# Kernel tuning notes

Hardware: AMD Instinct MI355X
Metric: run time of the kernel (lower is better)

## Reference

```python
import jax, jax.numpy as jnp
import numpy as np

B, T, D, N, H = 2, 2048, 1024, 16, 64
CAP = 50.0


def setup_inputs() -> dict:
    key = jax.random.key(0)
    ks = jax.random.split(key, 11)
    s_in = 1.0 / np.sqrt(D)   # kaiming_uniform(a=sqrt(5)) bound for fan_in=D
    s_out = 1.0 / np.sqrt(N * H)
    return {
        "q_vector": jax.random.normal(ks[0], (B, T, D), jnp.float32),
        "k_vector": jax.random.normal(ks[1], (B, T, D), jnp.float32),
        "v_vector": jax.random.normal(ks[2], (B, T, D), jnp.float32),
        "wq": jax.random.uniform(ks[3], (D, N, H), jnp.float32, -s_in, s_in),
        "bq": jnp.zeros((N, H), jnp.float32),
        "wk": jax.random.uniform(ks[4], (D, N, H), jnp.float32, -s_in, s_in),
        "bk": jnp.zeros((N, H), jnp.float32),
        "wv": jax.random.uniform(ks[5], (D, N, H), jnp.float32, -s_in, s_in),
        "bv": jnp.zeros((N, H), jnp.float32),
        "wo": jax.random.uniform(ks[6], (N, H, D), jnp.float32, -s_out, s_out),
        "bo": jnp.zeros((D,), jnp.float32),
    }


def reference(q_vector, k_vector, v_vector, wq, bq, wk, bk, wv, bv, wo, bo):
    # QKV projections: '...D,DNH->...NH' + bias
    q = jnp.einsum("btd,dnh->btnh", q_vector, wq) + bq
    k = jnp.einsum("bsd,dnh->bsnh", k_vector, wk) + bk
    v = jnp.einsum("bsd,dnh->bsnh", v_vector, wv) + bv
    # scale query by head_dim^-0.5 (use_per_dim_scale=False path)
    q = q * (H ** -0.5)
    # logits [B,N,T,S] with tanh soft-cap
    logits = jnp.einsum("btnh,bsnh->bnts", q, k)
    logits = CAP * jnp.tanh(logits / CAP)
    probs = jax.nn.softmax(logits, axis=-1)
    encoded = jnp.einsum("bnts,bsnh->btnh", probs, v)
    # output projection: '...NH,NHD->...D' + bias
    out = jnp.einsum("btnh,nhd->btd", encoded, wo) + bo
    return (out, probs)
```

## Files before the change

### kernel.cpp

```cpp
#include <hip/hip_runtime.h>

#define BB 2
#define TT 2048
#define DD 1024
#define NN 16
#define HH 64
#define NHC 1024
#define CAPV 50.0f

typedef float f32x4 __attribute__((ext_vector_type(4)));
typedef __bf16 bf16x8 __attribute__((ext_vector_type(8)));
typedef unsigned short u16x8 __attribute__((ext_vector_type(8)));

__device__ __forceinline__ unsigned short f2bf(float f) {
  unsigned u = __builtin_bit_cast(unsigned, f);
  unsigned r = (u + 0x7fffu + ((u >> 16) & 1u)) >> 16;
  return (unsigned short)r;
}

__device__ __forceinline__ void gld16(void* lds, const void* g) {
  __builtin_amdgcn_global_load_lds(
      (__attribute__((address_space(1))) void*)(const_cast<void*>(g)),
      (__attribute__((address_space(3))) void*)(lds), 16, 0, 0);
}

__global__ __launch_bounds__(256) void conv_inputs(
    const float* __restrict__ q, const float* __restrict__ k, const float* __restrict__ v,
    unsigned short* __restrict__ qo, unsigned short* __restrict__ ko, unsigned short* __restrict__ vo) {
  const float* src = blockIdx.z == 0 ? q : (blockIdx.z == 1 ? k : v);
  unsigned short* dst = blockIdx.z == 0 ? qo : (blockIdx.z == 1 ? ko : vo);
  size_t i = ((size_t)blockIdx.x * 256 + threadIdx.x) * 8;
  float4 a = *(const float4*)&src[i];
  float4 c = *(const float4*)&src[i + 4];
  u16x8 o;
  o[0] = f2bf(a.x); o[1] = f2bf(a.y); o[2] = f2bf(a.z); o[3] = f2bf(a.w);
  o[4] = f2bf(c.x); o[5] = f2bf(c.y); o[6] = f2bf(c.z); o[7] = f2bf(c.w);
  *(u16x8*)&dst[i] = o;
}

__global__ __launch_bounds__(256) void transpose_w(
    const float* __restrict__ wq, const float* __restrict__ wk,
    const float* __restrict__ wv, const float* __restrict__ wo,
    unsigned short* __restrict__ oq, unsigned short* __restrict__ ok,
    unsigned short* __restrict__ ov, unsigned short* __restrict__ oo) {
  __shared__ float tile[64][65];
  int z = blockIdx.z;
  const float* src = z == 0 ? wq : z == 1 ? wk : z == 2 ? wv : wo;
  unsigned short* dst = z == 0 ? oq : z == 1 ? ok : z == 2 ? ov : oo;
  int r0 = blockIdx.y * 64, c0 = blockIdx.x * 64;
  int tid = threadIdx.x;
#pragma unroll
  for (int i = 0; i < 16; ++i) {
    int idx = tid + 256 * i; int r = idx >> 6, c = idx & 63;
    tile[r][c] = src[(size_t)(r0 + r) * 1024 + c0 + c];
  }
  __syncthreads();
#pragma unroll
  for (int i = 0; i < 16; ++i) {
    int idx = tid + 256 * i; int rr = idx >> 6, cc = idx & 63;
    dst[(size_t)(c0 + rr) * 1024 + r0 + cc] = f2bf(tile[cc][rr]);
  }
}

__global__ __launch_bounds__(256) void transpose_v(
    const unsigned short* __restrict__ vb, unsigned short* __restrict__ vT) {
  __shared__ unsigned short tl[64][80];
  int s0 = blockIdx.x * 64, n = blockIdx.y, b = blockIdx.z;
  int tid = threadIdx.x;
  const size_t base = (size_t)b * TT * NHC + (size_t)n * HH;
#pragma unroll
  for (int i = 0; i < 2; ++i) {
    int c = tid + 256 * i; int r = c >> 3, g = c & 7;
    *(u16x8*)&tl[r][g * 8] = *(const u16x8*)&vb[base + (size_t)(s0 + r) * NHC + g * 8];
  }
  __syncthreads();
  const size_t vtb = (size_t)(b * NN + n) * HH * TT;
#pragma unroll
  for (int i = 0; i < 2; ++i) {
    int c = tid + 256 * i; int h = c >> 3, sg = c & 7;
    u16x8 w;
#pragma unroll
    for (int j = 0; j < 8; ++j) w[j] = tl[sg * 8 + j][h];
    *(u16x8*)&vT[vtb + (size_t)h * TT + s0 + sg * 8] = w;
  }
}

template <int OUT_F32>
__global__ __launch_bounds__(256) void gemm128(
    const unsigned short* __restrict__ A, const unsigned short* __restrict__ BT,
    const float* __restrict__ bias, void* __restrict__ Cout, float scale) {
  __shared__ unsigned short As[128 * 64];
  __shared__ unsigned short Bs[128 * 64];
  const int tid = threadIdx.x, lane = tid & 63, wave = tid >> 6;
  const int wm = wave >> 1, wn = wave & 1;
  const int l15 = lane & 15, l4 = lane >> 4;
  const int row0 = blockIdx.y * 128, col0 = blockIdx.x * 128;
  f32x4 acc[4][4] = {};
  for (int kt = 0; kt < 16; ++kt) {
    if (kt) __syncthreads();
#pragma unroll
    for (int i = 0; i < 4; ++i) {
      int c = tid + 256 * i; int r = c >> 3, g = (c & 7) ^ (r & 7);
      gld16(&As[c * 8], &A[(size_t)(row0 + r) * 1024 + kt * 64 + g * 8]);
    }
#pragma unroll
    for (int i = 0; i < 4; ++i) {
      int c = tid + 256 * i; int r = c >> 3, g = (c & 7) ^ (r & 7);
      gld16(&Bs[c * 8], &BT[(size_t)(col0 + r) * 1024 + kt * 64 + g * 8]);
    }
    __syncthreads();
#pragma unroll
    for (int ks = 0; ks < 2; ++ks) {
      bf16x8 af[4], bfr[4];
#pragma unroll
      for (int m = 0; m < 4; ++m) {
        int r = wm * 64 + m * 16 + l15;
        int ch = (ks * 4 + l4) ^ (r & 7);
        af[m] = *(const bf16x8*)&As[r * 64 + ch * 8];
      }
#pragma unroll
      for (int n = 0; n < 4; ++n) {
        int r = wn * 64 + n * 16 + l15;
        int ch = (ks * 4 + l4) ^ (r & 7);
        bfr[n] = *(const bf16x8*)&Bs[r * 64 + ch * 8];
      }
#pragma unroll
      for (int m = 0; m < 4; ++m)
#pragma unroll
        for (int n = 0; n < 4; ++n)
          acc[m][n] = __builtin_amdgcn_mfma_f32_16x16x32_bf16(af[m], bfr[n], acc[m][n], 0, 0, 0);
    }
  }
#pragma unroll
  for (int m = 0; m < 4; ++m)
#pragma unroll
    for (int n = 0; n < 4; ++n) {
      int col = col0 + wn * 64 + n * 16 + l15;
      float bv = bias[col];
#pragma unroll
      for (int r = 0; r < 4; ++r) {
        int row = row0 + wm * 64 + m * 16 + l4 * 4 + r;
        float v = (acc[m][n][r] + bv) * scale;
        if (OUT_F32) ((float*)Cout)[(size_t)row * 1024 + col] = v;
        else ((unsigned short*)Cout)[(size_t)row * 1024 + col] = f2bf(v);
      }
    }
}

__global__ __launch_bounds__(256) void attn_denom(
    const unsigned short* __restrict__ qb, const unsigned short* __restrict__ kb,
    float* __restrict__ denom) {
  __shared__ unsigned short q_lds[128 * 64];
  __shared__ unsigned short k_lds[128 * 64];
  __shared__ float rs[2][128];
  const int tid = threadIdx.x, lane = tid & 63, wave = tid >> 6;
  const int wm = wave >> 1, wn = wave & 1;
  const int l15 = lane & 15, l4 = lane >> 4;
  const int t0 = blockIdx.x * 128, n = blockIdx.y, b = blockIdx.z;
  const size_t base = (size_t)b * TT * NHC + (size_t)n * HH;
#pragma unroll
  for (int i = 0; i < 4; ++i) {
    int c = tid + 256 * i; int r = c >> 3, g = (c & 7) ^ (r & 7);
    gld16(&q_lds[c * 8], &qb[base + (size_t)(t0 + r) * NHC + g * 8]);
  }
  __syncthreads();
  bf16x8 qf[4][2];
#pragma unroll
  for (int m = 0; m < 4; ++m)
#pragma unroll
    for (int ks = 0; ks < 2; ++ks) {
      int r = wm * 64 + m * 16 + l15;
      int ch = (ks * 4 + l4) ^ (r & 7);
      qf[m][ks] = *(const bf16x8*)&q_lds[r * 64 + ch * 8];
    }
  float psum[4][4] = {};
  for (int st = 0; st < 16; ++st) {
    __syncthreads();
#pragma unroll
    for (int i = 0; i < 4; ++i) {
      int c = tid + 256 * i; int r = c >> 3, g = (c & 7) ^ (r & 7);
      gld16(&k_lds[c * 8], &kb[base + (size_t)(st * 128 + r) * NHC + g * 8]);
    }
    __syncthreads();
    f32x4 acc[4][4] = {};
#pragma unroll
    for (int ks = 0; ks < 2; ++ks) {
      bf16x8 bfr[4];
#pragma unroll
      for (int nf = 0; nf < 4; ++nf) {
        int r = wn * 64 + nf * 16 + l15;
        int ch = (ks * 4 + l4) ^ (r & 7);
        bfr[nf] = *(const bf16x8*)&k_lds[r * 64 + ch * 8];
      }
#pragma unroll
      for (int m = 0; m < 4; ++m)
#pragma unroll
        for (int nf = 0; nf < 4; ++nf)
          acc[m][nf] = __builtin_amdgcn_mfma_f32_16x16x32_bf16(qf[m][ks], bfr[nf], acc[m][nf], 0, 0, 0);
    }
#pragma unroll
    for (int m = 0; m < 4; ++m)
#pragma unroll
      for (int nf = 0; nf < 4; ++nf)
#pragma unroll
        for (int r = 0; r < 4; ++r) {
          float l = acc[m][nf][r];
          float u = __expf(l * (2.0f / CAPV));
          float ct = CAPV * (u - 1.0f) * __builtin_amdgcn_rcpf(u + 1.0f);
          psum[m][r] += __expf(ct);
        }
  }
#pragma unroll
  for (int m = 0; m < 4; ++m)
#pragma unroll
    for (int r = 0; r < 4; ++r) {
      float s = psum[m][r];
      s += __shfl_xor(s, 1);
      s += __shfl_xor(s, 2);
      s += __shfl_xor(s, 4);
      s += __shfl_xor(s, 8);
      if (l15 == 0) rs[wn][wm * 64 + m * 16 + l4 * 4 + r] = s;
    }
  __syncthreads();
  if (tid < 128) denom[((size_t)b * NN + n) * TT + t0 + tid] = rs[0][tid] + rs[1][tid];
}

__global__ __launch_bounds__(256) void attn_pv(
    const unsigned short* __restrict__ qb, const unsigned short* __restrict__ kb,
    const unsigned short* __restrict__ vT, const float* __restrict__ denom,
    float* __restrict__ probs, unsigned short* __restrict__ enc) {
  __shared__ unsigned short regA[64 * 128];
  __shared__ unsigned short regB[128 * 136];
  const int tid = threadIdx.x, lane = tid & 63, wave = tid >> 6;
  const int wm = wave >> 1, wn = wave & 1;
  const int l15 = lane & 15, l4 = lane >> 4;
  const int t0 = blockIdx.x * 128, n = blockIdx.y, b = blockIdx.z;
  const size_t base = (size_t)b * TT * NHC + (size_t)n * HH;
  const size_t vtb = (size_t)(b * NN + n) * HH * TT;
  const size_t prow = (size_t)(b * NN + n) * TT;
#pragma unroll
  for (int i = 0; i < 4; ++i) {
    int c = tid + 256 * i; int r = c >> 3, g = (c & 7) ^ (r & 7);
    gld16(&regA[c * 8], &qb[base + (size_t)(t0 + r) * NHC + g * 8]);
  }
  __syncthreads();
  bf16x8 qf[4][2];
#pragma unroll
  for (int m = 0; m < 4; ++m)
#pragma unroll
    for (int ks = 0; ks < 2; ++ks) {
      int r = wm * 64 + m * 16 + l15;
      int ch = (ks * 4 + l4) ^ (r & 7);
      qf[m][ks] = *(const bf16x8*)&regA[r * 64 + ch * 8];
    }
  float dinv[4][4];
#pragma unroll
  for (int m = 0; m < 4; ++m)
#pragma unroll
    for (int r = 0; r < 4; ++r)
      dinv[m][r] = 1.0f / denom[((size_t)b * NN + n) * TT + t0 + wm * 64 + m * 16 + l4 * 4 + r];
  __syncthreads();
  f32x4 eacc[2][4] = {};
  for (int st = 0; st < 16; ++st) {
    const int s0 = st * 128;
#pragma unroll
    for (int i = 0; i < 4; ++i) {
      int c = tid + 256 * i; int r = c >> 3, g = (c & 7) ^ (r & 7);
      gld16(&regB[c * 8], &kb[base + (size_t)(s0 + r) * NHC + g * 8]);
    }
#pragma unroll
    for (int i = 0; i < 4; ++i) {
      int c = tid + 256 * i; int h = c >> 4, g = (c & 15) ^ (h & 15);
      gld16(&regA[c * 8], &vT[vtb + (size_t)h * TT + s0 + g * 8]);
    }
    __syncthreads();
    f32x4 acc[4][4] = {};
#pragma unroll
    for (int ks = 0; ks < 2; ++ks) {
      bf16x8 bfr[4];
#pragma unroll
      for (int nf = 0; nf < 4; ++nf) {
        int r = wn * 64 + nf * 16 + l15;
        int ch = (ks * 4 + l4) ^ (r & 7);
        bfr[nf] = *(const bf16x8*)&regB[r * 64 + ch * 8];
      }
#pragma unroll
      for (int m = 0; m < 4; ++m)
#pragma unroll
        for (int nf = 0; nf < 4; ++nf)
          acc[m][nf] = __builtin_amdgcn_mfma_f32_16x16x32_bf16(qf[m][ks], bfr[nf], acc[m][nf], 0, 0, 0);
    }
    __syncthreads();
#pragma unroll
    for (int m = 0; m < 4; ++m)
#pragma unroll
      for (int nf = 0; nf < 4; ++nf) {
        int scol = wn * 64 + nf * 16 + l15;
#pragma unroll
        for (int r = 0; r < 4; ++r) {
          int trow = wm * 64 + m * 16 + l4 * 4 + r;
          float l = acc[m][nf][r];
          float u = __expf(l * (2.0f / CAPV));
          float ct = CAPV * (u - 1.0f) * __builtin_amdgcn_rcpf(u + 1.0f);
          float p = __expf(ct) * dinv[m][r];
          probs[(prow + t0 + trow) * (size_t)TT + s0 + scol] = p;
          regB[trow * 136 + scol] = f2bf(p);
        }
      }
    __syncthreads();
#pragma unroll
    for (int kst = 0; kst < 4; ++kst) {
      bf16x8 pa[2], vbf[4];
#pragma unroll
      for (int m2 = 0; m2 < 2; ++m2) {
        int t = wave * 32 + m2 * 16 + l15;
        pa[m2] = *(const bf16x8*)&regB[t * 136 + kst * 32 + l4 * 8];
      }
#pragma unroll
      for (int h4 = 0; h4 < 4; ++h4) {
        int h = h4 * 16 + l15;
        int ch = (kst * 4 + l4) ^ (h & 15);
        vbf[h4] = *(const bf16x8*)&regA[h * 128 + ch * 8];
      }
#pragma unroll
      for (int m2 = 0; m2 < 2; ++m2)
#pragma unroll
        for (int h4 = 0; h4 < 4; ++h4)
          eacc[m2][h4] = __builtin_amdgcn_mfma_f32_16x16x32_bf16(pa[m2], vbf[h4], eacc[m2][h4], 0, 0, 0);
    }
    __syncthreads();
  }
#pragma unroll
  for (int m2 = 0; m2 < 2; ++m2)
#pragma unroll
    for (int h4 = 0; h4 < 4; ++h4)
#pragma unroll
      for (int r = 0; r < 4; ++r) {
        int t = t0 + wave * 32 + m2 * 16 + l4 * 4 + r;
        int h = h4 * 16 + l15;
        enc[base + (size_t)t * NHC + h] = f2bf(eacc[m2][h4][r]);
      }
}

extern "C" void kernel_launch(void* const* d_in, const int* in_sizes, int n_in,
                              void* d_out, int out_size, void* d_ws, size_t ws_size,
                              hipStream_t stream) {
  const float* qv = (const float*)d_in[0];
  const float* kv = (const float*)d_in[1];
  const float* vv = (const float*)d_in[2];
  const float* wq = (const float*)d_in[3];
  const float* bq = (const float*)d_in[4];
  const float* wk = (const float*)d_in[5];
  const float* bk = (const float*)d_in[6];
  const float* wv = (const float*)d_in[7];
  const float* bv = (const float*)d_in[8];
  const float* wo = (const float*)d_in[9];
  const float* bo = (const float*)d_in[10];
  char* ws = (char*)d_ws;
  unsigned short* qb   = (unsigned short*)(ws + 0);
  unsigned short* kb   = (unsigned short*)(ws + 8388608);
  unsigned short* vb   = (unsigned short*)(ws + 16777216);
  unsigned short* vTb  = (unsigned short*)(ws + 25165824);
  unsigned short* wqT  = (unsigned short*)(ws + 33554432);
  unsigned short* wkT  = (unsigned short*)(ws + 35651584);
  unsigned short* wvT  = (unsigned short*)(ws + 37748736);
  unsigned short* woT  = (unsigned short*)(ws + 39845888);
  unsigned short* qinb = (unsigned short*)(ws + 41943040);
  unsigned short* kinb = (unsigned short*)(ws + 50331648);
  unsigned short* vinb = (unsigned short*)(ws + 58720256);
  float* denom         = (float*)(ws + 67108864);
  unsigned short* enc  = (unsigned short*)(ws + 67371008);

  float* out = (float*)d_out;
  float* probs = out + (size_t)BB * TT * DD;

  conv_inputs<<<dim3(2048, 1, 3), 256, 0, stream>>>(qv, kv, vv, qinb, kinb, vinb);
  transpose_w<<<dim3(16, 16, 4), 256, 0, stream>>>(wq, wk, wv, wo, wqT, wkT, wvT, woT);
  gemm128<0><<<dim3(8, 32), 256, 0, stream>>>(qinb, wqT, bq, qb, 0.125f);
  gemm128<0><<<dim3(8, 32), 256, 0, stream>>>(kinb, wkT, bk, kb, 1.0f);
  gemm128<0><<<dim3(8, 32), 256, 0, stream>>>(vinb, wvT, bv, vb, 1.0f);
  transpose_v<<<dim3(32, 16, 2), 256, 0, stream>>>(vb, vTb);
  attn_denom<<<dim3(16, 16, 2), 256, 0, stream>>>(qb, kb, denom);
  attn_pv<<<dim3(16, 16, 2), 256, 0, stream>>>(qb, kb, vTb, denom, probs, enc);
  gemm128<1><<<dim3(8, 32), 256, 0, stream>>>(enc, woT, bo, out, 1.0f);
}
```

Baseline: 368.8 us.

## Fuse denominator and PV attention kernels into one sync-free per-wave kernel

Merges the two attention kernels into one launch, with a block-index remap for locality. Each wave owns 32 query rows and recomputes QK^T twice: once for the softmax denominator, once for the probabilities and PV product. K and V fragments are read straight from global memory instead of staged through shared memory, which removes all block barriers. Probabilities are packed to bf16 in a small per-wave LDS tile and written back as 16-byte vector stores, and the normalisation moves to the encoder output. The trade-offs are redundant global K/V reads across waves, and probs now derived from bf16-rounded values, which costs some precision.

```diff
diff --git a/kernel.cpp b/kernel.cpp
--- a/kernel.cpp
+++ b/kernel.cpp
@@ -147,61 +147,51 @@
     }
 }
 
-__global__ __launch_bounds__(256) void attn_denom(
+__global__ __launch_bounds__(256, 2) void fused_attn(
     const unsigned short* __restrict__ qb, const unsigned short* __restrict__ kb,
-    float* __restrict__ denom) {
-  __shared__ unsigned short q_lds[128 * 64];
-  __shared__ unsigned short k_lds[128 * 64];
-  __shared__ float rs[2][128];
+    const unsigned short* __restrict__ vT, float* __restrict__ probs,
+    unsigned short* __restrict__ enc) {
+  __shared__ unsigned short P_lds[4][32][136];
   const int tid = threadIdx.x, lane = tid & 63, wave = tid >> 6;
-  const int wm = wave >> 1, wn = wave & 1;
   const int l15 = lane & 15, l4 = lane >> 4;
-  const int t0 = blockIdx.x * 128, n = blockIdx.y, b = blockIdx.z;
+  const int bid = blockIdx.x;
+  const int logical = (bid & 7) * 64 + (bid >> 3);
+  const int bt = logical & 15, head = logical >> 4;
+  const int n = head & 15, b = head >> 4;
+  const int t0 = bt * 128;
+  const int wrow0 = t0 + wave * 32;
   const size_t base = (size_t)b * TT * NHC + (size_t)n * HH;
-#pragma unroll
-  for (int i = 0; i < 4; ++i) {
-    int c = tid + 256 * i; int r = c >> 3, g = (c & 7) ^ (r & 7);
-    gld16(&q_lds[c * 8], &qb[base + (size_t)(t0 + r) * NHC + g * 8]);
-  }
-  __syncthreads();
-  bf16x8 qf[4][2];
-#pragma unroll
-  for (int m = 0; m < 4; ++m)
+  const size_t vtb = (size_t)(b * NN + n) * HH * TT;
+  const size_t prow = (size_t)(b * NN + n) * TT;
+
+  bf16x8 qf[2][2];
+#pragma unroll
+  for (int m = 0; m < 2; ++m)
+#pragma unroll
+    for (int ks = 0; ks < 2; ++ks)
+      qf[m][ks] = *(const bf16x8*)&qb[base + (size_t)(wrow0 + m * 16 + l15) * NHC + ks * 32 + l4 * 8];
+
+  float psum[2][4] = {};
+#pragma unroll 1
+  for (int st = 0; st < 16; ++st) {
+    const int s0 = st * 128;
+    f32x4 acc[2][8] = {};
 #pragma unroll
     for (int ks = 0; ks < 2; ++ks) {
-      int r = wm * 64 + m * 16 + l15;
-      int ch = (ks * 4 + l4) ^ (r & 7);
-      qf[m][ks] = *(const bf16x8*)&q_lds[r * 64 + ch * 8];
-    }
-  float psum[4][4] = {};
-  for (int st = 0; st < 16; ++st) {
-    __syncthreads();
-#pragma unroll
-    for (int i = 0; i < 4; ++i) {
-      int c = tid + 256 * i; int r = c >> 3, g = (c & 7) ^ (r & 7);
-      gld16(&k_lds[c * 8], &kb[base + (size_t)(st * 128 + r) * NHC + g * 8]);
-    }
-    __syncthreads();
-    f32x4 acc[4][4] = {};
-#pragma unroll
-    for (int ks = 0; ks < 2; ++ks) {
-      bf16x8 bfr[4];
-#pragma unroll
-      for (int nf = 0; nf < 4; ++nf) {
-        int r = wn * 64 + nf * 16 + l15;
-        int ch = (ks * 4 + l4) ^ (r & 7);
-        bfr[nf] = *(const bf16x8*)&k_lds[r * 64 + ch * 8];
-      }
-#pragma unroll
-      for (int m = 0; m < 4; ++m)
-#pragma unroll
-        for (int nf = 0; nf < 4; ++nf)
-          acc[m][nf] = __builtin_amdgcn_mfma_f32_16x16x32_bf16(qf[m][ks], bfr[nf], acc[m][nf], 0, 0, 0);
-    }
-#pragma unroll
-    for (int m = 0; m < 4; ++m)
-#pragma unroll
-      for (int nf = 0; nf < 4; ++nf)
+      bf16x8 kf[8];
+#pragma unroll
+      for (int nf = 0; nf < 8; ++nf)
+        kf[nf] = *(const bf16x8*)&kb[base + (size_t)(s0 + nf * 16 + l15) * NHC + ks * 32 + l4 * 8];
+#pragma unroll
+      for (int m = 0; m < 2; ++m)
+#pragma unroll
+        for (int nf = 0; nf < 8; ++nf)
+          acc[m][nf] = __builtin_amdgcn_mfma_f32_16x16x32_bf16(qf[m][ks], kf[nf], acc[m][nf], 0, 0, 0);
+    }
+#pragma unroll
+    for (int m = 0; m < 2; ++m)
+#pragma unroll
+      for (int nf = 0; nf < 8; ++nf)
 #pragma unroll
         for (int r = 0; r < 4; ++r) {
           float l = acc[m][nf][r];
@@ -210,8 +200,9 @@
           psum[m][r] += __expf(ct);
         }
   }
-#pragma unroll
-  for (int m = 0; m < 4; ++m)
+  float dinv[2][4];
+#pragma unroll
+  for (int m = 0; m < 2; ++m)
 #pragma unroll
     for (int r = 0; r < 4; ++r) {
       float s = psum[m][r];
@@ -219,126 +210,93 @@
       s += __shfl_xor(s, 2);
       s += __shfl_xor(s, 4);
       s += __shfl_xor(s, 8);
-      if (l15 == 0) rs[wn][wm * 64 + m * 16 + l4 * 4 + r] = s;
-    }
-  __syncthreads();
-  if (tid < 128) denom[((size_t)b * NN + n) * TT + t0 + tid] = rs[0][tid] + rs[1][tid];
-}
-
-__global__ __launch_bounds__(256) void attn_pv(
-    const unsigned short* __restrict__ qb, const unsigned short* __restrict__ kb,
-    const unsigned short* __restrict__ vT, const float* __restrict__ denom,
-    float* __restrict__ probs, unsigned short* __restrict__ enc) {
-  __shared__ unsigned short regA[64 * 128];
-  __shared__ unsigned short regB[128 * 136];
-  const int tid = threadIdx.x, lane = tid & 63, wave = tid >> 6;
-  const int wm = wave >> 1, wn = wave & 1;
-  const int l15 = lane & 15, l4 = lane >> 4;
-  const int t0 = blockIdx.x * 128, n = blockIdx.y, b = blockIdx.z;
-  const size_t base = (size_t)b * TT * NHC + (size_t)n * HH;
-  const size_t vtb = (size_t)(b * NN + n) * HH * TT;
-  const size_t prow = (size_t)(b * NN + n) * TT;
-#pragma unroll
-  for (int i = 0; i < 4; ++i) {
-    int c = tid + 256 * i; int r = c >> 3, g = (c & 7) ^ (r & 7);
-    gld16(&regA[c * 8], &qb[base + (size_t)(t0 + r) * NHC + g * 8]);
-  }
-  __syncthreads();
-  bf16x8 qf[4][2];
-#pragma unroll
-  for (int m = 0; m < 4; ++m)
-#pragma unroll
-    for (int ks = 0; ks < 2; ++ks) {
-      int r = wm * 64 + m * 16 + l15;
-      int ch = (ks * 4 + l4) ^ (r & 7);
-      qf[m][ks] = *(const bf16x8*)&regA[r * 64 + ch * 8];
-    }
-  float dinv[4][4];
-#pragma unroll
-  for (int m = 0; m < 4; ++m)
-#pragma unroll
-    for (int r = 0; r < 4; ++r)
-      dinv[m][r] = 1.0f / denom[((size_t)b * NN + n) * TT + t0 + wm * 64 + m * 16 + l4 * 4 + r];
-  __syncthreads();
+      dinv[m][r] = 1.0f / s;
+    }
+
   f32x4 eacc[2][4] = {};
+#pragma unroll 1
   for (int st = 0; st < 16; ++st) {
     const int s0 = st * 128;
-#pragma unroll
-    for (int i = 0; i < 4; ++i) {
-      int c = tid + 256 * i; int r = c >> 3, g = (c & 7) ^ (r & 7);
-      gld16(&regB[c * 8], &kb[base + (size_t)(s0 + r) * NHC + g * 8]);
-    }
-#pragma unroll
-    for (int i = 0; i < 4; ++i) {
-      int c = tid + 256 * i; int h = c >> 4, g = (c & 15) ^ (h & 15);
-      gld16(&regA[c * 8], &vT[vtb + (size_t)h * TT + s0 + g * 8]);
-    }
-    __syncthreads();
-    f32x4 acc[4][4] = {};
+    f32x4 acc[2][8] = {};
 #pragma unroll
     for (int ks = 0; ks < 2; ++ks) {
-      bf16x8 bfr[4];
-#pragma unroll
-      for (int nf = 0; nf < 4; ++nf) {
-        int r = wn * 64 + nf * 16 + l15;
-        int ch = (ks * 4 + l4) ^ (r & 7);
-        bfr[nf] = *(const bf16x8*)&regB[r * 64 + ch * 8];
-      }
-#pragma unroll
-      for (int m = 0; m < 4; ++m)
-#pragma unroll
-        for (int nf = 0; nf < 4; ++nf)
-          acc[m][nf] = __builtin_amdgcn_mfma_f32_16x16x32_bf16(qf[m][ks], bfr[nf], acc[m][nf], 0, 0, 0);
-    }
-    __syncthreads();
-#pragma unroll
-    for (int m = 0; m < 4; ++m)
-#pragma unroll
-      for (int nf = 0; nf < 4; ++nf) {
-        int scol = wn * 64 + nf * 16 + l15;
-#pragma unroll
-        for (int r = 0; r < 4; ++r) {
-          int trow = wm * 64 + m * 16 + l4 * 4 + r;
+      bf16x8 kf[8];
+#pragma unroll
+      for (int nf = 0; nf < 8; ++nf)
+        kf[nf] = *(const bf16x8*)&kb[base + (size_t)(s0 + nf * 16 + l15) * NHC + ks * 32 + l4 * 8];
+#pragma unroll
+      for (int m = 0; m < 2; ++m)
+#pragma unroll
+        for (int nf = 0; nf < 8; ++nf)
+          acc[m][nf] = __builtin_amdgcn_mfma_f32_16x16x32_bf16(qf[m][ks], kf[nf], acc[m][nf], 0, 0, 0);
+    }
+    const bool evl = (l15 & 1) == 0;
+#pragma unroll
+    for (int m = 0; m < 2; ++m)
+#pragma unroll
+      for (int r = 0; r < 4; ++r) {
+        float ev[8], pw[8];
+#pragma unroll
+        for (int nf = 0; nf < 8; ++nf) {
           float l = acc[m][nf][r];
           float u = __expf(l * (2.0f / CAPV));
           float ct = CAPV * (u - 1.0f) * __builtin_amdgcn_rcpf(u + 1.0f);
-          float p = __expf(ct) * dinv[m][r];
-          probs[(prow + t0 + trow) * (size_t)TT + s0 + scol] = p;
-          regB[trow * 136 + scol] = f2bf(p);
+          ev[nf] = __expf(ct);
         }
-      }
-    __syncthreads();
+#pragma unroll
+        for (int nf = 0; nf < 8; ++nf) pw[nf] = __shfl_xor(ev[nf], 1);
+        const int row = m * 16 + l4 * 4 + r;
+        unsigned short* Pr = &P_lds[wave][row][0];
+#pragma unroll
+        for (int j = 0; j < 4; ++j) {
+          float lo = evl ? ev[j] : pw[j + 4];
+          float hi = evl ? pw[j] : ev[j + 4];
+          unsigned pk;
+          asm("v_cvt_pk_bf16_f32 %0, %1, %2" : "=v"(pk) : "v"(lo), "v"(hi));
+          int col = (evl ? j * 16 : (j + 4) * 16) + (l15 & ~1);
+          *(unsigned*)&Pr[col] = pk;
+        }
+      }
+    asm volatile("s_waitcnt lgkmcnt(0)" ::: "memory");
+#pragma unroll
+    for (int m = 0; m < 2; ++m)
+#pragma unroll
+      for (int r = 0; r < 4; ++r) {
+        const int row = m * 16 + l4 * 4 + r;
+        bf16x8 p8 = *(const bf16x8*)&P_lds[wave][row][l15 * 8];
+        float dv = dinv[m][r];
+        f32x4 o0, o1;
+#pragma unroll
+        for (int j = 0; j < 4; ++j) { o0[j] = (float)p8[j] * dv; o1[j] = (float)p8[j + 4] * dv; }
+        size_t off = (prow + (size_t)(wrow0 + row)) * TT + s0 + l15 * 8;
+        *(f32x4*)&probs[off] = o0;
+        *(f32x4*)&probs[off + 4] = o1;
+      }
 #pragma unroll
     for (int kst = 0; kst < 4; ++kst) {
-      bf16x8 pa[2], vbf[4];
-#pragma unroll
-      for (int m2 = 0; m2 < 2; ++m2) {
-        int t = wave * 32 + m2 * 16 + l15;
-        pa[m2] = *(const bf16x8*)&regB[t * 136 + kst * 32 + l4 * 8];
-      }
-#pragma unroll
-      for (int h4 = 0; h4 < 4; ++h4) {
+      bf16x8 pa[2], vf[4];
+#pragma unroll
+      for (int m2 = 0; m2 < 2; ++m2)
+        pa[m2] = *(const bf16x8*)&P_lds[wave][m2 * 16 + l15][kst * 32 + l4 * 8];
+#pragma unroll
+      for (int h4 = 0; h4 < 4; ++h4)
+        vf[h4] = *(const bf16x8*)&vT[vtb + (size_t)(h4 * 16 + l15) * TT + s0 + kst * 32 + l4 * 8];
+#pragma unroll
+      for (int m2 = 0; m2 < 2; ++m2)
+#pragma unroll
+        for (int h4 = 0; h4 < 4; ++h4)
+          eacc[m2][h4] = __builtin_amdgcn_mfma_f32_16x16x32_bf16(pa[m2], vf[h4], eacc[m2][h4], 0, 0, 0);
+    }
+  }
+#pragma unroll
+  for (int m2 = 0; m2 < 2; ++m2)
+#pragma unroll
+    for (int h4 = 0; h4 < 4; ++h4)
+#pragma unroll
+      for (int r = 0; r < 4; ++r) {
+        int t = wrow0 + m2 * 16 + l4 * 4 + r;
         int h = h4 * 16 + l15;
-        int ch = (kst * 4 + l4) ^ (h & 15);
-        vbf[h4] = *(const bf16x8*)&regA[h * 128 + ch * 8];
-      }
-#pragma unroll
-      for (int m2 = 0; m2 < 2; ++m2)
-#pragma unroll
-        for (int h4 = 0; h4 < 4; ++h4)
-          eacc[m2][h4] = __builtin_amdgcn_mfma_f32_16x16x32_bf16(pa[m2], vbf[h4], eacc[m2][h4], 0, 0, 0);
-    }
-    __syncthreads();
-  }
-#pragma unroll
-  for (int m2 = 0; m2 < 2; ++m2)
-#pragma unroll
-    for (int h4 = 0; h4 < 4; ++h4)
-#pragma unroll
-      for (int r = 0; r < 4; ++r) {
-        int t = t0 + wave * 32 + m2 * 16 + l4 * 4 + r;
-        int h = h4 * 16 + l15;
-        enc[base + (size_t)t * NHC + h] = f2bf(eacc[m2][h4][r]);
+        enc[base + (size_t)t * NHC + h] = f2bf(eacc[m2][h4][r] * dinv[m2][r]);
       }
 }
 
@@ -368,7 +326,6 @@
   unsigned short* qinb = (unsigned short*)(ws + 41943040);
   unsigned short* kinb = (unsigned short*)(ws + 50331648);
   unsigned short* vinb = (unsigned short*)(ws + 58720256);
-  float* denom         = (float*)(ws + 67108864);
   unsigned short* enc  = (unsigned short*)(ws + 67371008);
 
   float* out = (float*)d_out;
@@ -380,7 +337,6 @@
   gemm128<0><<<dim3(8, 32), 256, 0, stream>>>(kinb, wkT, bk, kb, 1.0f);
   gemm128<0><<<dim3(8, 32), 256, 0, stream>>>(vinb, wvT, bv, vb, 1.0f);
   transpose_v<<<dim3(32, 16, 2), 256, 0, stream>>>(vb, vTb);
-  attn_denom<<<dim3(16, 16, 2), 256, 0, stream>>>(qb, kb, denom);
-  attn_pv<<<dim3(16, 16, 2), 256, 0, stream>>>(qb, kb, vTb, denom, probs, enc);
+  fused_attn<<<dim3(512), 256, 0, stream>>>(qb, kb, vTb, probs, enc);
   gemm128<1><<<dim3(8, 32), 256, 0, stream>>>(enc, woT, bo, out, 1.0f);
 }
```

Result: slower. 428.0 us (+16.1%).
